# Kernel tuning notes

Hardware: AMD Instinct MI355X
Metric: run time of the kernel (lower is better)

The kernel has to match this reference:

```python
import jax, jax.numpy as jnp
import numpy as np

N_NODES = 50000


def gcn_conv(x, edge_index, W, b, n):
    # PyG GCNConv: xW, add self-loops, symmetric degree normalization,
    # scatter-add messages from source (row) to target (col).
    xw = x @ W
    row, col = edge_index[0], edge_index[1]
    loops = jnp.arange(n, dtype=edge_index.dtype)
    row = jnp.concatenate([row, loops])
    col = jnp.concatenate([col, loops])
    deg = jax.ops.segment_sum(jnp.ones(row.shape[0], dtype=xw.dtype), col, num_segments=n)
    dinv = jnp.where(deg > 0, jax.lax.rsqrt(deg), 0.0)
    norm = dinv[row] * dinv[col]  # [E+N]
    out = jax.ops.segment_sum(xw[row] * norm[:, None], col, num_segments=n)
    return out + b


def setup_inputs() -> dict:
    key = jax.random.key(0)
    ks = jax.random.split(key, 5)
    n, d_in, d_h, d_out, n_edges = N_NODES, 128, 128, 4, 600000
    x = jax.random.normal(ks[0], (n, d_in), dtype=jnp.float32)
    edge_index = jax.random.randint(ks[1], (2, n_edges), 0, n, dtype=jnp.int64)
    W1 = jax.random.normal(ks[2], (d_in, d_h), dtype=jnp.float32) * (1.0 / np.sqrt(d_in))
    b1 = jnp.zeros((d_h,), dtype=jnp.float32)
    W2 = jax.random.normal(ks[3], (d_h, d_h), dtype=jnp.float32) * (1.0 / np.sqrt(d_h))
    b2 = jnp.zeros((d_h,), dtype=jnp.float32)
    Wfc = jax.random.normal(ks[4], (2 * d_h, d_out), dtype=jnp.float32) * (1.0 / np.sqrt(2 * d_h))
    bfc = jnp.zeros((d_out,), dtype=jnp.float32)
    return {"x": x, "edge_index": edge_index, "W1": W1, "b1": b1,
            "W2": W2, "b2": b2, "Wfc": Wfc, "bfc": bfc}


def reference(x, edge_index, W1, b1, W2, b2, Wfc, bfc):
    n = x.shape[0]
    # dropout is identity at inference (training=False)
    h = jax.nn.relu(gcn_conv(x, edge_index, W1, b1, n))
    h = jax.nn.relu(gcn_conv(h, edge_index, W2, b2, n))
    # edge-level gather + concat + linear classifier
    edge_x = jnp.concatenate([h[edge_index[0]], h[edge_index[1]]], axis=-1)  # [E, 2*d_h]
    edge_scores = edge_x @ Wfc + bfc  # [E, d_out]
    return jax.nn.log_softmax(edge_scores, axis=1)
```

## Files before the change

### kernel.cpp

```cpp
#include <hip/hip_runtime.h>
#include <math.h>
#include <stdint.h>

#define D 128
#define SCAN_CHUNK 2048
#define LDA 136

typedef __attribute__((ext_vector_type(8))) short v8s;
typedef __attribute__((ext_vector_type(4))) float v4f;

static __device__ __forceinline__ uint16_t f2bf(float f) {
    uint32_t u = __float_as_uint(f);
    u = (u + 0x7fff + ((u >> 16) & 1)) >> 16;
    return (uint16_t)u;
}
static __device__ __forceinline__ float bf2f(uint16_t h) { return __uint_as_float((uint32_t)h << 16); }
static __device__ __forceinline__ float bf_lo(uint32_t u) { return __uint_as_float(u << 16); }
static __device__ __forceinline__ float bf_hi(uint32_t u) { return __uint_as_float(u & 0xffff0000u); }


__global__ void countpack_kernel(const int* __restrict__ col, int* __restrict__ cnt,
                                 int* __restrict__ rnk, int E,
                                 const float* __restrict__ W1, const float* __restrict__ W2,
                                 uint16_t* __restrict__ Wh, uint16_t* __restrict__ Wl) {
    int tid = blockIdx.x * blockDim.x + threadIdx.x;
    if (tid < 2 * 16384) {
        int layer = tid >> 14;
        int li = tid & 16383;
        int j = li & 7, lane = (li >> 3) & 63, f = li >> 9;
        int kstep = f >> 3, tile = f & 7;
        int k = kstep * 32 + ((lane >> 4) * 8) + j;
        int nn = tile * 16 + (lane & 15);
        const float* W = layer ? W2 : W1;
        float v = W[k * 128 + nn];
        uint16_t h = f2bf(v);
        Wh[tid] = h;
        Wl[tid] = f2bf(v - bf2f(h));
    }
    if (tid < E) rnk[tid] = atomicAdd(&cnt[col[tid]], 1);
}


__global__ __launch_bounds__(256) void scanA_kernel(const int* __restrict__ cnt,
                                                    int* __restrict__ bsum,
                                                    float* __restrict__ dinv, int n) {
    __shared__ int wsum[4];
    int b = blockIdx.x, t = threadIdx.x;
    int base = b * SCAN_CHUNK;
    int s = 0;
#pragma unroll
    for (int k = 0; k < SCAN_CHUNK / 256; k++) {
        int i = base + k * 256 + t;
        if (i < n) {
            int c = cnt[i];
            s += c;
            dinv[i] = rsqrtf((float)c + 1.0f);
        }
    }
#pragma unroll
    for (int off = 32; off > 0; off >>= 1) s += __shfl_xor(s, off, 64);
    if ((t & 63) == 0) wsum[t >> 6] = s;
    __syncthreads();
    if (t == 0) bsum[b] = wsum[0] + wsum[1] + wsum[2] + wsum[3];
}


__global__ __launch_bounds__(256) void scanC_kernel(const int* __restrict__ cnt,
                                                    const int* __restrict__ bsum,
                                                    int* __restrict__ offs, int n, int nb) {
    __shared__ int stage[SCAN_CHUNK];
    __shared__ int res[SCAN_CHUNK];
    __shared__ int tsum[256];
    __shared__ int sb[64];
    int b = blockIdx.x, t = threadIdx.x;
    if (t < 64) {
        int v = (t < nb) ? bsum[t] : 0;
        int inc = v;
#pragma unroll
        for (int off = 1; off < 64; off <<= 1) {
            int u = __shfl_up(inc, off, 64);
            if (t >= off) inc += u;
        }
        sb[t] = inc;
    }
    int base = b * SCAN_CHUNK;
#pragma unroll
    for (int k = 0; k < SCAN_CHUNK / 256; k++) {
        int i = base + k * 256 + t;
        stage[k * 256 + t] = (i < n) ? cnt[i] : 0;
    }
    __syncthreads();
    int my = 0;
#pragma unroll
    for (int j = 0; j < 8; j++) my += stage[t * 8 + j];
    tsum[t] = my;
    __syncthreads();
    for (int off = 1; off < 256; off <<= 1) {
        int v = (t >= off) ? tsum[t - off] : 0;
        __syncthreads();
        tsum[t] += v;
        __syncthreads();
    }
    int bbase = (b == 0) ? 0 : sb[b - 1];
    int run = tsum[t] - my + bbase;
#pragma unroll
    for (int j = 0; j < 8; j++) {
        res[t * 8 + j] = run;
        run += stage[t * 8 + j];
    }
    __syncthreads();
#pragma unroll
    for (int k = 0; k < SCAN_CHUNK / 256; k++) {
        int i = base + k * 256 + t;
        if (i < n) offs[i] = res[k * 256 + t];
    }
    if (b == gridDim.x - 1 && t == 0) offs[n] = sb[nb - 1];
}


static __device__ __forceinline__ void gemm_body(const uint16_t Ah[][LDA],
                                                 const uint16_t Al[][LDA],
                                                 const uint16_t* __restrict__ Wph,
                                                 const uint16_t* __restrict__ Wpl,
                                                 const float* __restrict__ dinv,
                                                 uint16_t* __restrict__ Cb,
                                                 int base_row, int M, int t) {
    int lane = t & 63, w = t >> 6;
    int m_l = lane & 15, quad = lane >> 4;
    int arow = w * 16 + m_l;

    v4f acc[8];
#pragma unroll
    for (int i = 0; i < 8; i++) acc[i] = (v4f){0.f, 0.f, 0.f, 0.f};

#pragma unroll
    for (int ks = 0; ks < 4; ks++) {
        v8s ah = *(const v8s*)&Ah[arow][ks * 32 + quad * 8];
        v8s al = *(const v8s*)&Al[arow][ks * 32 + quad * 8];
#pragma unroll
        for (int ti = 0; ti < 8; ti++) {
            int f = ks * 8 + ti;
            v8s bh = *(const v8s*)(Wph + ((size_t)(f * 64 + lane)) * 8);
            v8s bl = *(const v8s*)(Wpl + ((size_t)(f * 64 + lane)) * 8);
            acc[ti] = __builtin_amdgcn_mfma_f32_16x16x32_bf16(al, bh, acc[ti], 0, 0, 0);
            acc[ti] = __builtin_amdgcn_mfma_f32_16x16x32_bf16(ah, bl, acc[ti], 0, 0, 0);
            acc[ti] = __builtin_amdgcn_mfma_f32_16x16x32_bf16(ah, bh, acc[ti], 0, 0, 0);
        }
    }

    int rbase = base_row + w * 16 + quad * 4;
#pragma unroll
    for (int reg = 0; reg < 4; reg++) {
        int gr = rbase + reg;
        if (gr < M) {
            float di = dinv[gr];
#pragma unroll
            for (int ti = 0; ti < 8; ti++) {
                Cb[(size_t)gr * D + ti * 16 + m_l] = f2bf(di * acc[ti][reg]);
            }
        }
    }
}


__global__ __launch_bounds__(256) void fillgemm_kernel(const int* __restrict__ row,
                                                       const int* __restrict__ col,
                                                       const int* __restrict__ rnk,
                                                       const int* __restrict__ offs,
                                                       int* __restrict__ adj, int E,
                                                       const float* __restrict__ A,
                                                       const uint16_t* __restrict__ Wph,
                                                       const uint16_t* __restrict__ Wpl,
                                                       const float* __restrict__ dinv,
                                                       uint16_t* __restrict__ Cb, int M,
                                                       int nbG) {
    __shared__ uint16_t Ah[64][LDA];
    __shared__ uint16_t Al[64][LDA];
    int t = threadIdx.x;

    if (blockIdx.x >= nbG) {
        int e = (blockIdx.x - nbG) * 256 + t;
        if (e < E) adj[offs[col[e]] + rnk[e]] = row[e];
        return;
    }

    int base_row = blockIdx.x * 64;
#pragma unroll
    for (int kk = 0; kk < 8; kk++) {
        int idx = kk * 256 + t;
        int r = idx >> 5;
        int c4 = idx & 31;
        int gr = base_row + r;
        float4 f = (gr < M) ? *(const float4*)(A + (size_t)gr * D + c4 * 4)
                            : make_float4(0.f, 0.f, 0.f, 0.f);
        uint16_t h0 = f2bf(f.x), h1 = f2bf(f.y), h2 = f2bf(f.z), h3 = f2bf(f.w);
        uint16_t l0 = f2bf(f.x - bf2f(h0)), l1 = f2bf(f.y - bf2f(h1));
        uint16_t l2 = f2bf(f.z - bf2f(h2)), l3 = f2bf(f.w - bf2f(h3));
        *(ushort4*)&Ah[r][c4 * 4] = make_ushort4(h0, h1, h2, h3);
        *(ushort4*)&Al[r][c4 * 4] = make_ushort4(l0, l1, l2, l3);
    }
    __syncthreads();
    gemm_body(Ah, Al, Wph, Wpl, dinv, Cb, base_row, M, t);
}


__global__ __launch_bounds__(256) void agggemm_kernel(const uint32_t* __restrict__ xwb,
                                                      const int* __restrict__ adj,
                                                      const int* __restrict__ offs,
                                                      const float* __restrict__ dinv,
                                                      const float* __restrict__ bias,
                                                      const uint16_t* __restrict__ Wph,
                                                      const uint16_t* __restrict__ Wpl,
                                                      uint16_t* __restrict__ Cb, int M) {
    __shared__ uint16_t Ah[64][LDA];
    __shared__ uint16_t Al[64][LDA];
    int t = threadIdx.x, lane = t & 63, w = t >> 6;
    int base_row = blockIdx.x * 64;
    float2 bv = ((const float2*)bias)[lane];

    for (int rr = 0; rr < 8; rr++) {
        int rA = w * 16 + rr, rB = rA + 8;
        int iA = base_row + rA, iB = base_row + rB;
        float a0 = 0.f, a1 = 0.f, c0 = 0.f, c1 = 0.f;
        int jA = 0, eA = 0, jB = 0, eB = 0;
        if (iA < M) {
            uint32_t su = xwb[(size_t)iA * (D / 2) + lane];
            a0 = bf_lo(su); a1 = bf_hi(su);
            jA = offs[iA]; eA = offs[iA + 1];
        }
        if (iB < M) {
            uint32_t su = xwb[(size_t)iB * (D / 2) + lane];
            c0 = bf_lo(su); c1 = bf_hi(su);
            jB = offs[iB]; eB = offs[iB + 1];
        }
        while (jA + 7 < eA && jB + 7 < eB) {
            int xx[8], yy[8];
#pragma unroll
            for (int q = 0; q < 8; q++) { xx[q] = adj[jA + q]; yy[q] = adj[jB + q]; }
            uint32_t uA[8], uB[8];
#pragma unroll
            for (int q = 0; q < 8; q++) {
                uA[q] = xwb[(size_t)xx[q] * (D / 2) + lane];
                uB[q] = xwb[(size_t)yy[q] * (D / 2) + lane];
            }
#pragma unroll
            for (int q = 0; q < 8; q++) {
                a0 += bf_lo(uA[q]); a1 += bf_hi(uA[q]);
                c0 += bf_lo(uB[q]); c1 += bf_hi(uB[q]);
            }
            jA += 8; jB += 8;
        }
        for (; jA + 7 < eA; jA += 8) {
            int xx[8]; uint32_t uA[8];
#pragma unroll
            for (int q = 0; q < 8; q++) xx[q] = adj[jA + q];
#pragma unroll
            for (int q = 0; q < 8; q++) uA[q] = xwb[(size_t)xx[q] * (D / 2) + lane];
#pragma unroll
            for (int q = 0; q < 8; q++) { a0 += bf_lo(uA[q]); a1 += bf_hi(uA[q]); }
        }
        for (; jA + 3 < eA; jA += 4) {
            int x0 = adj[jA], x1 = adj[jA + 1], x2 = adj[jA + 2], x3 = adj[jA + 3];
            uint32_t u0 = xwb[(size_t)x0 * (D / 2) + lane];
            uint32_t u1 = xwb[(size_t)x1 * (D / 2) + lane];
            uint32_t u2 = xwb[(size_t)x2 * (D / 2) + lane];
            uint32_t u3 = xwb[(size_t)x3 * (D / 2) + lane];
            a0 += bf_lo(u0); a1 += bf_hi(u0);
            a0 += bf_lo(u1); a1 += bf_hi(u1);
            a0 += bf_lo(u2); a1 += bf_hi(u2);
            a0 += bf_lo(u3); a1 += bf_hi(u3);
        }
        for (; jA < eA; jA++) {
            uint32_t u = xwb[(size_t)adj[jA] * (D / 2) + lane];
            a0 += bf_lo(u); a1 += bf_hi(u);
        }
        for (; jB + 7 < eB; jB += 8) {
            int yy[8]; uint32_t uB[8];
#pragma unroll
            for (int q = 0; q < 8; q++) yy[q] = adj[jB + q];
#pragma unroll
            for (int q = 0; q < 8; q++) uB[q] = xwb[(size_t)yy[q] * (D / 2) + lane];
#pragma unroll
            for (int q = 0; q < 8; q++) { c0 += bf_lo(uB[q]); c1 += bf_hi(uB[q]); }
        }
        for (; jB + 3 < eB; jB += 4) {
            int y0 = adj[jB], y1 = adj[jB + 1], y2 = adj[jB + 2], y3 = adj[jB + 3];
            uint32_t u0 = xwb[(size_t)y0 * (D / 2) + lane];
            uint32_t u1 = xwb[(size_t)y1 * (D / 2) + lane];
            uint32_t u2 = xwb[(size_t)y2 * (D / 2) + lane];
            uint32_t u3 = xwb[(size_t)y3 * (D / 2) + lane];
            c0 += bf_lo(u0); c1 += bf_hi(u0);
            c0 += bf_lo(u1); c1 += bf_hi(u1);
            c0 += bf_lo(u2); c1 += bf_hi(u2);
            c0 += bf_lo(u3); c1 += bf_hi(u3);
        }
        for (; jB < eB; jB++) {
            uint32_t u = xwb[(size_t)adj[jB] * (D / 2) + lane];
            c0 += bf_lo(u); c1 += bf_hi(u);
        }
        float diA = (iA < M) ? dinv[iA] : 0.f;
        float diB = (iB < M) ? dinv[iB] : 0.f;
        float oA0 = fmaxf(fmaf(diA, a0, bv.x), 0.f);
        float oA1 = fmaxf(fmaf(diA, a1, bv.y), 0.f);
        float oB0 = fmaxf(fmaf(diB, c0, bv.x), 0.f);
        float oB1 = fmaxf(fmaf(diB, c1, bv.y), 0.f);
        if (iA >= M) { oA0 = 0.f; oA1 = 0.f; }
        if (iB >= M) { oB0 = 0.f; oB1 = 0.f; }
        uint16_t hA0 = f2bf(oA0), hA1 = f2bf(oA1);
        uint16_t lA0 = f2bf(oA0 - bf2f(hA0)), lA1 = f2bf(oA1 - bf2f(hA1));
        uint16_t hB0 = f2bf(oB0), hB1 = f2bf(oB1);
        uint16_t lB0 = f2bf(oB0 - bf2f(hB0)), lB1 = f2bf(oB1 - bf2f(hB1));
        *(ushort2*)&Ah[rA][2 * lane] = make_ushort2(hA0, hA1);
        *(ushort2*)&Al[rA][2 * lane] = make_ushort2(lA0, lA1);
        *(ushort2*)&Ah[rB][2 * lane] = make_ushort2(hB0, hB1);
        *(ushort2*)&Al[rB][2 * lane] = make_ushort2(lB0, lB1);
    }
    __syncthreads();
    gemm_body(Ah, Al, Wph, Wpl, dinv, Cb, base_row, M, t);
}


__global__ __launch_bounds__(256) void agg2pq_kernel(const uint32_t* __restrict__ xwb,
                                                     const int* __restrict__ adj,
                                                     const int* __restrict__ offs,
                                                     const float* __restrict__ dinv,
                                                     const float* __restrict__ bias,
                                                     const float* __restrict__ Wfc,
                                                     const float* __restrict__ bfc,
                                                     float* __restrict__ P1,
                                                     float* __restrict__ P2, int n) {
    int wave = (int)((blockIdx.x * (size_t)blockDim.x + threadIdx.x) >> 6);
    int lane = threadIdx.x & 63;
    if (wave >= n) return;
    int i = wave;
    uint32_t su = xwb[(size_t)i * (D / 2) + lane];
    float acc0 = bf_lo(su);
    float acc1 = bf_hi(su);
    int s = offs[i], e = offs[i + 1];
    int j = s;
    for (; j + 7 < e; j += 8) {
        int r0 = adj[j],     r1 = adj[j + 1], r2 = adj[j + 2], r3 = adj[j + 3];
        int r4 = adj[j + 4], r5 = adj[j + 5], r6 = adj[j + 6], r7 = adj[j + 7];
        uint32_t u0 = xwb[(size_t)r0 * (D / 2) + lane];
        uint32_t u1 = xwb[(size_t)r1 * (D / 2) + lane];
        uint32_t u2 = xwb[(size_t)r2 * (D / 2) + lane];
        uint32_t u3 = xwb[(size_t)r3 * (D / 2) + lane];
        uint32_t u4 = xwb[(size_t)r4 * (D / 2) + lane];
        uint32_t u5 = xwb[(size_t)r5 * (D / 2) + lane];
        uint32_t u6 = xwb[(size_t)r6 * (D / 2) + lane];
        uint32_t u7 = xwb[(size_t)r7 * (D / 2) + lane];
        acc0 += bf_lo(u0); acc1 += bf_hi(u0);
        acc0 += bf_lo(u1); acc1 += bf_hi(u1);
        acc0 += bf_lo(u2); acc1 += bf_hi(u2);
        acc0 += bf_lo(u3); acc1 += bf_hi(u3);
        acc0 += bf_lo(u4); acc1 += bf_hi(u4);
        acc0 += bf_lo(u5); acc1 += bf_hi(u5);
        acc0 += bf_lo(u6); acc1 += bf_hi(u6);
        acc0 += bf_lo(u7); acc1 += bf_hi(u7);
    }
    for (; j + 3 < e; j += 4) {
        int r0 = adj[j], r1 = adj[j + 1], r2 = adj[j + 2], r3 = adj[j + 3];
        uint32_t u0 = xwb[(size_t)r0 * (D / 2) + lane];
        uint32_t u1 = xwb[(size_t)r1 * (D / 2) + lane];
        uint32_t u2 = xwb[(size_t)r2 * (D / 2) + lane];
        uint32_t u3 = xwb[(size_t)r3 * (D / 2) + lane];
        acc0 += bf_lo(u0); acc1 += bf_hi(u0);
        acc0 += bf_lo(u1); acc1 += bf_hi(u1);
        acc0 += bf_lo(u2); acc1 += bf_hi(u2);
        acc0 += bf_lo(u3); acc1 += bf_hi(u3);
    }
    for (; j < e; j++) {
        int r = adj[j];
        uint32_t u = xwb[(size_t)r * (D / 2) + lane];
        acc0 += bf_lo(u); acc1 += bf_hi(u);
    }
    float di = dinv[i];
    float2 bv = ((const float2*)bias)[lane];
    float o0 = fmaxf(fmaf(di, acc0, bv.x), 0.f);
    float o1 = fmaxf(fmaf(di, acc1, bv.y), 0.f);

    const float4* W4 = (const float4*)Wfc;
    float4 wa = W4[2 * lane];
    float4 wb = W4[2 * lane + 1];
    float4 wc = W4[128 + 2 * lane];
    float4 wd = W4[129 + 2 * lane];
    float p0 = fmaf(o0, wa.x, o1 * wb.x), p1 = fmaf(o0, wa.y, o1 * wb.y);
    float p2 = fmaf(o0, wa.z, o1 * wb.z), p3 = fmaf(o0, wa.w, o1 * wb.w);
    float q0 = fmaf(o0, wc.x, o1 * wd.x), q1 = fmaf(o0, wc.y, o1 * wd.y);
    float q2 = fmaf(o0, wc.z, o1 * wd.z), q3 = fmaf(o0, wc.w, o1 * wd.w);
#pragma unroll
    for (int off = 1; off < 64; off <<= 1) {
        p0 += __shfl_xor(p0, off, 64);
        p1 += __shfl_xor(p1, off, 64);
        p2 += __shfl_xor(p2, off, 64);
        p3 += __shfl_xor(p3, off, 64);
        q0 += __shfl_xor(q0, off, 64);
        q1 += __shfl_xor(q1, off, 64);
        q2 += __shfl_xor(q2, off, 64);
        q3 += __shfl_xor(q3, off, 64);
    }
    if (lane == 0) {
        float4 bb = *(const float4*)bfc;
        *(float4*)(P1 + (size_t)i * 4) = make_float4(p0 + bb.x, p1 + bb.y, p2 + bb.z, p3 + bb.w);
        *(float4*)(P2 + (size_t)i * 4) = make_float4(q0, q1, q2, q3);
    }
}


__global__ __launch_bounds__(256) void edge2_kernel(const int* __restrict__ row,
                                                    const int* __restrict__ col,
                                                    const float* __restrict__ P1,
                                                    const float* __restrict__ P2,
                                                    float* __restrict__ out, int E) {
    int e = blockIdx.x * blockDim.x + threadIdx.x;
    if (e >= E) return;
    int r = row[e], c = col[e];
    float4 a = ((const float4*)P1)[r];
    float4 b = ((const float4*)P2)[c];
    float sx = a.x + b.x, sy = a.y + b.y, sz = a.z + b.z, sw = a.w + b.w;
    float m = fmaxf(fmaxf(sx, sy), fmaxf(sz, sw));
    float e0 = expf(sx - m), e1 = expf(sy - m), e2 = expf(sz - m), e3 = expf(sw - m);
    float lse = m + logf(e0 + e1 + e2 + e3);
    *(float4*)(out + (size_t)e * 4) = make_float4(sx - lse, sy - lse, sz - lse, sw - lse);
}


extern "C" void kernel_launch(void* const* d_in, const int* in_sizes, int n_in,
                              void* d_out, int out_size, void* d_ws, size_t ws_size,
                              hipStream_t stream) {
    const float* x   = (const float*)d_in[0];
    const int*   ei  = (const int*)d_in[1];
    const float* W1  = (const float*)d_in[2];
    const float* b1  = (const float*)d_in[3];
    const float* W2  = (const float*)d_in[4];
    const float* b2  = (const float*)d_in[5];
    const float* Wfc = (const float*)d_in[6];
    const float* bfc = (const float*)d_in[7];
    float* out = (float*)d_out;

    int n = in_sizes[0] / D;
    int E = in_sizes[1] / 2;
    const int* row = ei;
    const int* col = ei + E;

    int nbScan = (n + SCAN_CHUNK - 1) / SCAN_CHUNK;

    uint16_t* xwb  = (uint16_t*)d_ws;
    uint16_t* xwb2 = xwb + (size_t)n * D;
    int*      cnt  = (int*)(xwb2 + (size_t)n * D);
    int*      offs = cnt + n;
    int*      bsum = offs + (n + 4);
    int*      adj  = bsum + 64;
    int*      rnk  = adj + E;
    float*    dinv = (float*)(rnk + E);
    uint16_t* Wph  = (uint16_t*)(dinv + n);
    uint16_t* Wpl  = Wph + 2 * 16384;
    float*    P1   = (float*)(Wpl + 2 * 16384);
    float*    P2   = P1 + (size_t)n * 4;

    int nb_e = (E + 255) / 256;
    int nbG  = (n + 63) / 64;

    hipMemsetAsync(cnt, 0, (size_t)n * sizeof(int), stream);
    countpack_kernel<<<nb_e, 256, 0, stream>>>(col, cnt, rnk, E, W1, W2, Wph, Wpl);
    scanA_kernel<<<nbScan, 256, 0, stream>>>(cnt, bsum, dinv, n);
    scanC_kernel<<<nbScan, 256, 0, stream>>>(cnt, bsum, offs, n, nbScan);

    fillgemm_kernel<<<nbG + nb_e, 256, 0, stream>>>(row, col, rnk, offs, adj, E,
                                                    x, Wph, Wpl, dinv, xwb, n, nbG);

    agggemm_kernel<<<nbG, 256, 0, stream>>>((const uint32_t*)xwb, adj, offs, dinv, b1,
                                            Wph + 16384, Wpl + 16384, xwb2, n);

    agg2pq_kernel<<<(n + 3) / 4, 256, 0, stream>>>((const uint32_t*)xwb2, adj, offs, dinv, b2,
                                                   Wfc, bfc, P1, P2, n);

    edge2_kernel<<<nb_e, 256, 0, stream>>>(row, col, P1, P2, out, E);
}
```

Baseline: 235.7 us.

## Split feature dimension into quarter tables for cache-local gather aggregation

The GEMM output changes to a quarter-blocked layout of four 32-column slabs, each n×32 bf16, so each aggregation pass gathers from a smaller table that fits in L2 cache. Aggregation splits into persistent grid-stride kernels, with block index mapped to a quarter. Layer 1 aggregation now writes fp32 h1 to a separate buffer, and a standalone gemm2 kernel consumes it. Layer 2 aggregation accumulates the classifier projections into P1/P2 with atomics, after scanA pre-initialises them with the bias and zeros. This adds an fp32 intermediate round trip, an extra launch and atomic traffic, in exchange for better gather locality.

```diff
diff --git a/kernel.cpp b/kernel.cpp
--- a/kernel.cpp
+++ b/kernel.cpp
@@ -5,6 +5,8 @@
 #define D 128
 #define SCAN_CHUNK 2048
 #define LDA 136
+#define AGG_BLOCKS 4096
+#define AGG_STRIDE 4096
 
 typedef __attribute__((ext_vector_type(8))) short v8s;
 typedef __attribute__((ext_vector_type(4))) float v4f;
@@ -43,10 +45,14 @@
 
 __global__ __launch_bounds__(256) void scanA_kernel(const int* __restrict__ cnt,
                                                     int* __restrict__ bsum,
-                                                    float* __restrict__ dinv, int n) {
+                                                    float* __restrict__ dinv,
+                                                    const float* __restrict__ bfc,
+                                                    float* __restrict__ P1,
+                                                    float* __restrict__ P2, int n) {
     __shared__ int wsum[4];
     int b = blockIdx.x, t = threadIdx.x;
     int base = b * SCAN_CHUNK;
+    float4 bb = *(const float4*)bfc;
     int s = 0;
 #pragma unroll
     for (int k = 0; k < SCAN_CHUNK / 256; k++) {
@@ -55,6 +61,8 @@
             int c = cnt[i];
             s += c;
             dinv[i] = rsqrtf((float)c + 1.0f);
+            ((float4*)P1)[i] = bb;
+            ((float4*)P2)[i] = make_float4(0.f, 0.f, 0.f, 0.f);
         }
     }
 #pragma unroll
@@ -156,7 +164,8 @@
             float di = dinv[gr];
 #pragma unroll
             for (int ti = 0; ti < 8; ti++) {
-                Cb[(size_t)gr * D + ti * 16 + m_l] = f2bf(di * acc[ti][reg]);
+                Cb[(((size_t)(ti >> 1)) * M + gr) * 32 + (ti & 1) * 16 + m_l] =
+                    f2bf(di * acc[ti][reg]);
             }
         }
     }
@@ -204,205 +213,151 @@
 }
 
 
-__global__ __launch_bounds__(256) void agggemm_kernel(const uint32_t* __restrict__ xwb,
-                                                      const int* __restrict__ adj,
-                                                      const int* __restrict__ offs,
-                                                      const float* __restrict__ dinv,
-                                                      const float* __restrict__ bias,
-                                                      const uint16_t* __restrict__ Wph,
-                                                      const uint16_t* __restrict__ Wpl,
-                                                      uint16_t* __restrict__ Cb, int M) {
+__global__ __launch_bounds__(256) void gemm2_kernel(const float* __restrict__ h1q,
+                                                    const uint16_t* __restrict__ Wph,
+                                                    const uint16_t* __restrict__ Wpl,
+                                                    const float* __restrict__ dinv,
+                                                    uint16_t* __restrict__ Cb, int M) {
     __shared__ uint16_t Ah[64][LDA];
     __shared__ uint16_t Al[64][LDA];
-    int t = threadIdx.x, lane = t & 63, w = t >> 6;
+    int t = threadIdx.x;
     int base_row = blockIdx.x * 64;
-    float2 bv = ((const float2*)bias)[lane];
-
-    for (int rr = 0; rr < 8; rr++) {
-        int rA = w * 16 + rr, rB = rA + 8;
-        int iA = base_row + rA, iB = base_row + rB;
-        float a0 = 0.f, a1 = 0.f, c0 = 0.f, c1 = 0.f;
-        int jA = 0, eA = 0, jB = 0, eB = 0;
-        if (iA < M) {
-            uint32_t su = xwb[(size_t)iA * (D / 2) + lane];
-            a0 = bf_lo(su); a1 = bf_hi(su);
-            jA = offs[iA]; eA = offs[iA + 1];
-        }
-        if (iB < M) {
-            uint32_t su = xwb[(size_t)iB * (D / 2) + lane];
-            c0 = bf_lo(su); c1 = bf_hi(su);
-            jB = offs[iB]; eB = offs[iB + 1];
-        }
-        while (jA + 7 < eA && jB + 7 < eB) {
-            int xx[8], yy[8];
-#pragma unroll
-            for (int q = 0; q < 8; q++) { xx[q] = adj[jA + q]; yy[q] = adj[jB + q]; }
-            uint32_t uA[8], uB[8];
-#pragma unroll
-            for (int q = 0; q < 8; q++) {
-                uA[q] = xwb[(size_t)xx[q] * (D / 2) + lane];
-                uB[q] = xwb[(size_t)yy[q] * (D / 2) + lane];
-            }
-#pragma unroll
-            for (int q = 0; q < 8; q++) {
-                a0 += bf_lo(uA[q]); a1 += bf_hi(uA[q]);
-                c0 += bf_lo(uB[q]); c1 += bf_hi(uB[q]);
-            }
-            jA += 8; jB += 8;
-        }
-        for (; jA + 7 < eA; jA += 8) {
-            int xx[8]; uint32_t uA[8];
-#pragma unroll
-            for (int q = 0; q < 8; q++) xx[q] = adj[jA + q];
-#pragma unroll
-            for (int q = 0; q < 8; q++) uA[q] = xwb[(size_t)xx[q] * (D / 2) + lane];
-#pragma unroll
-            for (int q = 0; q < 8; q++) { a0 += bf_lo(uA[q]); a1 += bf_hi(uA[q]); }
-        }
-        for (; jA + 3 < eA; jA += 4) {
-            int x0 = adj[jA], x1 = adj[jA + 1], x2 = adj[jA + 2], x3 = adj[jA + 3];
-            uint32_t u0 = xwb[(size_t)x0 * (D / 2) + lane];
-            uint32_t u1 = xwb[(size_t)x1 * (D / 2) + lane];
-            uint32_t u2 = xwb[(size_t)x2 * (D / 2) + lane];
-            uint32_t u3 = xwb[(size_t)x3 * (D / 2) + lane];
-            a0 += bf_lo(u0); a1 += bf_hi(u0);
+#pragma unroll
+    for (int kk = 0; kk < 8; kk++) {
+        int idx = kk * 256 + t;
+        int r = idx >> 5;
+        int c4 = idx & 31;
+        int gr = base_row + r;
+        int qq = c4 >> 3, cc = c4 & 7;
+        float4 f = (gr < M) ? ((const float4*)h1q)[((size_t)qq * M + gr) * 8 + cc]
+                            : make_float4(0.f, 0.f, 0.f, 0.f);
+        uint16_t h0 = f2bf(f.x), h1 = f2bf(f.y), h2 = f2bf(f.z), h3 = f2bf(f.w);
+        uint16_t l0 = f2bf(f.x - bf2f(h0)), l1 = f2bf(f.y - bf2f(h1));
+        uint16_t l2 = f2bf(f.z - bf2f(h2)), l3 = f2bf(f.w - bf2f(h3));
+        *(ushort4*)&Ah[r][c4 * 4] = make_ushort4(h0, h1, h2, h3);
+        *(ushort4*)&Al[r][c4 * 4] = make_ushort4(l0, l1, l2, l3);
+    }
+    __syncthreads();
+    gemm_body(Ah, Al, Wph, Wpl, dinv, Cb, base_row, M, t);
+}
+
+
+__global__ __launch_bounds__(256) void aggq1_kernel(const uint32_t* __restrict__ xwbq,
+                                                    const int* __restrict__ adj,
+                                                    const int* __restrict__ offs,
+                                                    const float* __restrict__ dinv,
+                                                    const float* __restrict__ bias,
+                                                    float* __restrict__ h1q, int n) {
+    int b = blockIdx.x, t = threadIdx.x;
+    int q = (b & 7) >> 1;
+    int sub = ((b >> 3) << 1) + (b & 1);
+    int w = t >> 6, lane = t & 63;
+    int c = lane & 15, e = lane >> 4;
+    const uint32_t* tbl = xwbq + (size_t)q * n * 16;
+    float2 bv = ((const float2*)bias)[q * 16 + c];
+    for (int i = sub * 4 + w; i < n; i += AGG_STRIDE) {
+        uint32_t su = tbl[(size_t)i * 16 + c];
+        float a0 = (e == 0) ? bf_lo(su) : 0.f;
+        float a1 = (e == 0) ? bf_hi(su) : 0.f;
+        int j = offs[i], en = offs[i + 1];
+        for (; j + 7 < en; j += 8) {
+            int i1 = adj[j + e], i2 = adj[j + 4 + e];
+            uint32_t u1 = tbl[(size_t)i1 * 16 + c];
+            uint32_t u2 = tbl[(size_t)i2 * 16 + c];
+            a0 += bf_lo(u1) + bf_lo(u2);
+            a1 += bf_hi(u1) + bf_hi(u2);
+        }
+        for (; j + 3 < en; j += 4) {
+            int i1 = adj[j + e];
+            uint32_t u1 = tbl[(size_t)i1 * 16 + c];
             a0 += bf_lo(u1); a1 += bf_hi(u1);
-            a0 += bf_lo(u2); a1 += bf_hi(u2);
-            a0 += bf_lo(u3); a1 += bf_hi(u3);
-        }
-        for (; jA < eA; jA++) {
-            uint32_t u = xwb[(size_t)adj[jA] * (D / 2) + lane];
-            a0 += bf_lo(u); a1 += bf_hi(u);
-        }
-        for (; jB + 7 < eB; jB += 8) {
-            int yy[8]; uint32_t uB[8];
-#pragma unroll
-            for (int q = 0; q < 8; q++) yy[q] = adj[jB + q];
-#pragma unroll
-            for (int q = 0; q < 8; q++) uB[q] = xwb[(size_t)yy[q] * (D / 2) + lane];
-#pragma unroll
-            for (int q = 0; q < 8; q++) { c0 += bf_lo(uB[q]); c1 += bf_hi(uB[q]); }
-        }
-        for (; jB + 3 < eB; jB += 4) {
-            int y0 = adj[jB], y1 = adj[jB + 1], y2 = adj[jB + 2], y3 = adj[jB + 3];
-            uint32_t u0 = xwb[(size_t)y0 * (D / 2) + lane];
-            uint32_t u1 = xwb[(size_t)y1 * (D / 2) + lane];
-            uint32_t u2 = xwb[(size_t)y2 * (D / 2) + lane];
-            uint32_t u3 = xwb[(size_t)y3 * (D / 2) + lane];
-            c0 += bf_lo(u0); c1 += bf_hi(u0);
-            c0 += bf_lo(u1); c1 += bf_hi(u1);
-            c0 += bf_lo(u2); c1 += bf_hi(u2);
-            c0 += bf_lo(u3); c1 += bf_hi(u3);
-        }
-        for (; jB < eB; jB++) {
-            uint32_t u = xwb[(size_t)adj[jB] * (D / 2) + lane];
-            c0 += bf_lo(u); c1 += bf_hi(u);
-        }
-        float diA = (iA < M) ? dinv[iA] : 0.f;
-        float diB = (iB < M) ? dinv[iB] : 0.f;
-        float oA0 = fmaxf(fmaf(diA, a0, bv.x), 0.f);
-        float oA1 = fmaxf(fmaf(diA, a1, bv.y), 0.f);
-        float oB0 = fmaxf(fmaf(diB, c0, bv.x), 0.f);
-        float oB1 = fmaxf(fmaf(diB, c1, bv.y), 0.f);
-        if (iA >= M) { oA0 = 0.f; oA1 = 0.f; }
-        if (iB >= M) { oB0 = 0.f; oB1 = 0.f; }
-        uint16_t hA0 = f2bf(oA0), hA1 = f2bf(oA1);
-        uint16_t lA0 = f2bf(oA0 - bf2f(hA0)), lA1 = f2bf(oA1 - bf2f(hA1));
-        uint16_t hB0 = f2bf(oB0), hB1 = f2bf(oB1);
-        uint16_t lB0 = f2bf(oB0 - bf2f(hB0)), lB1 = f2bf(oB1 - bf2f(hB1));
-        *(ushort2*)&Ah[rA][2 * lane] = make_ushort2(hA0, hA1);
-        *(ushort2*)&Al[rA][2 * lane] = make_ushort2(lA0, lA1);
-        *(ushort2*)&Ah[rB][2 * lane] = make_ushort2(hB0, hB1);
-        *(ushort2*)&Al[rB][2 * lane] = make_ushort2(lB0, lB1);
-    }
-    __syncthreads();
-    gemm_body(Ah, Al, Wph, Wpl, dinv, Cb, base_row, M, t);
-}
-
-
-__global__ __launch_bounds__(256) void agg2pq_kernel(const uint32_t* __restrict__ xwb,
-                                                     const int* __restrict__ adj,
-                                                     const int* __restrict__ offs,
-                                                     const float* __restrict__ dinv,
-                                                     const float* __restrict__ bias,
-                                                     const float* __restrict__ Wfc,
-                                                     const float* __restrict__ bfc,
-                                                     float* __restrict__ P1,
-                                                     float* __restrict__ P2, int n) {
-    int wave = (int)((blockIdx.x * (size_t)blockDim.x + threadIdx.x) >> 6);
-    int lane = threadIdx.x & 63;
-    if (wave >= n) return;
-    int i = wave;
-    uint32_t su = xwb[(size_t)i * (D / 2) + lane];
-    float acc0 = bf_lo(su);
-    float acc1 = bf_hi(su);
-    int s = offs[i], e = offs[i + 1];
-    int j = s;
-    for (; j + 7 < e; j += 8) {
-        int r0 = adj[j],     r1 = adj[j + 1], r2 = adj[j + 2], r3 = adj[j + 3];
-        int r4 = adj[j + 4], r5 = adj[j + 5], r6 = adj[j + 6], r7 = adj[j + 7];
-        uint32_t u0 = xwb[(size_t)r0 * (D / 2) + lane];
-        uint32_t u1 = xwb[(size_t)r1 * (D / 2) + lane];
-        uint32_t u2 = xwb[(size_t)r2 * (D / 2) + lane];
-        uint32_t u3 = xwb[(size_t)r3 * (D / 2) + lane];
-        uint32_t u4 = xwb[(size_t)r4 * (D / 2) + lane];
-        uint32_t u5 = xwb[(size_t)r5 * (D / 2) + lane];
-        uint32_t u6 = xwb[(size_t)r6 * (D / 2) + lane];
-        uint32_t u7 = xwb[(size_t)r7 * (D / 2) + lane];
-        acc0 += bf_lo(u0); acc1 += bf_hi(u0);
-        acc0 += bf_lo(u1); acc1 += bf_hi(u1);
-        acc0 += bf_lo(u2); acc1 += bf_hi(u2);
-        acc0 += bf_lo(u3); acc1 += bf_hi(u3);
-        acc0 += bf_lo(u4); acc1 += bf_hi(u4);
-        acc0 += bf_lo(u5); acc1 += bf_hi(u5);
-        acc0 += bf_lo(u6); acc1 += bf_hi(u6);
-        acc0 += bf_lo(u7); acc1 += bf_hi(u7);
-    }
-    for (; j + 3 < e; j += 4) {
-        int r0 = adj[j], r1 = adj[j + 1], r2 = adj[j + 2], r3 = adj[j + 3];
-        uint32_t u0 = xwb[(size_t)r0 * (D / 2) + lane];
-        uint32_t u1 = xwb[(size_t)r1 * (D / 2) + lane];
-        uint32_t u2 = xwb[(size_t)r2 * (D / 2) + lane];
-        uint32_t u3 = xwb[(size_t)r3 * (D / 2) + lane];
-        acc0 += bf_lo(u0); acc1 += bf_hi(u0);
-        acc0 += bf_lo(u1); acc1 += bf_hi(u1);
-        acc0 += bf_lo(u2); acc1 += bf_hi(u2);
-        acc0 += bf_lo(u3); acc1 += bf_hi(u3);
-    }
-    for (; j < e; j++) {
-        int r = adj[j];
-        uint32_t u = xwb[(size_t)r * (D / 2) + lane];
-        acc0 += bf_lo(u); acc1 += bf_hi(u);
-    }
-    float di = dinv[i];
-    float2 bv = ((const float2*)bias)[lane];
-    float o0 = fmaxf(fmaf(di, acc0, bv.x), 0.f);
-    float o1 = fmaxf(fmaf(di, acc1, bv.y), 0.f);
-
+        }
+        if (j + e < en) {
+            uint32_t u1 = tbl[(size_t)adj[j + e] * 16 + c];
+            a0 += bf_lo(u1); a1 += bf_hi(u1);
+        }
+        a0 += __shfl_xor(a0, 16, 64); a0 += __shfl_xor(a0, 32, 64);
+        a1 += __shfl_xor(a1, 16, 64); a1 += __shfl_xor(a1, 32, 64);
+        float di = dinv[i];
+        float o0 = fmaxf(fmaf(di, a0, bv.x), 0.f);
+        float o1 = fmaxf(fmaf(di, a1, bv.y), 0.f);
+        if (lane < 16)
+            ((float2*)h1q)[((size_t)q * n + i) * 16 + c] = make_float2(o0, o1);
+    }
+}
+
+
+__global__ __launch_bounds__(256) void aggq2_kernel(const uint32_t* __restrict__ xwbq,
+                                                    const int* __restrict__ adj,
+                                                    const int* __restrict__ offs,
+                                                    const float* __restrict__ dinv,
+                                                    const float* __restrict__ bias,
+                                                    const float* __restrict__ Wfc,
+                                                    float* __restrict__ P1,
+                                                    float* __restrict__ P2, int n) {
+    int b = blockIdx.x, t = threadIdx.x;
+    int q = (b & 7) >> 1;
+    int sub = ((b >> 3) << 1) + (b & 1);
+    int w = t >> 6, lane = t & 63;
+    int c = lane & 15, e = lane >> 4;
+    const uint32_t* tbl = xwbq + (size_t)q * n * 16;
+    float2 bv = ((const float2*)bias)[q * 16 + c];
     const float4* W4 = (const float4*)Wfc;
-    float4 wa = W4[2 * lane];
-    float4 wb = W4[2 * lane + 1];
-    float4 wc = W4[128 + 2 * lane];
-    float4 wd = W4[129 + 2 * lane];
-    float p0 = fmaf(o0, wa.x, o1 * wb.x), p1 = fmaf(o0, wa.y, o1 * wb.y);
-    float p2 = fmaf(o0, wa.z, o1 * wb.z), p3 = fmaf(o0, wa.w, o1 * wb.w);
-    float q0 = fmaf(o0, wc.x, o1 * wd.x), q1 = fmaf(o0, wc.y, o1 * wd.y);
-    float q2 = fmaf(o0, wc.z, o1 * wd.z), q3 = fmaf(o0, wc.w, o1 * wd.w);
-#pragma unroll
-    for (int off = 1; off < 64; off <<= 1) {
-        p0 += __shfl_xor(p0, off, 64);
-        p1 += __shfl_xor(p1, off, 64);
-        p2 += __shfl_xor(p2, off, 64);
-        p3 += __shfl_xor(p3, off, 64);
-        q0 += __shfl_xor(q0, off, 64);
-        q1 += __shfl_xor(q1, off, 64);
-        q2 += __shfl_xor(q2, off, 64);
-        q3 += __shfl_xor(q3, off, 64);
-    }
-    if (lane == 0) {
-        float4 bb = *(const float4*)bfc;
-        *(float4*)(P1 + (size_t)i * 4) = make_float4(p0 + bb.x, p1 + bb.y, p2 + bb.z, p3 + bb.w);
-        *(float4*)(P2 + (size_t)i * 4) = make_float4(q0, q1, q2, q3);
+    float4 w1a = W4[q * 32 + 2 * c];
+    float4 w1b = W4[q * 32 + 2 * c + 1];
+    float4 w2a = W4[128 + q * 32 + 2 * c];
+    float4 w2b = W4[128 + q * 32 + 2 * c + 1];
+    for (int i = sub * 4 + w; i < n; i += AGG_STRIDE) {
+        uint32_t su = tbl[(size_t)i * 16 + c];
+        float a0 = (e == 0) ? bf_lo(su) : 0.f;
+        float a1 = (e == 0) ? bf_hi(su) : 0.f;
+        int j = offs[i], en = offs[i + 1];
+        for (; j + 7 < en; j += 8) {
+            int i1 = adj[j + e], i2 = adj[j + 4 + e];
+            uint32_t u1 = tbl[(size_t)i1 * 16 + c];
+            uint32_t u2 = tbl[(size_t)i2 * 16 + c];
+            a0 += bf_lo(u1) + bf_lo(u2);
+            a1 += bf_hi(u1) + bf_hi(u2);
+        }
+        for (; j + 3 < en; j += 4) {
+            int i1 = adj[j + e];
+            uint32_t u1 = tbl[(size_t)i1 * 16 + c];
+            a0 += bf_lo(u1); a1 += bf_hi(u1);
+        }
+        if (j + e < en) {
+            uint32_t u1 = tbl[(size_t)adj[j + e] * 16 + c];
+            a0 += bf_lo(u1); a1 += bf_hi(u1);
+        }
+        a0 += __shfl_xor(a0, 16, 64); a0 += __shfl_xor(a0, 32, 64);
+        a1 += __shfl_xor(a1, 16, 64); a1 += __shfl_xor(a1, 32, 64);
+        float di = dinv[i];
+        float o0 = fmaxf(fmaf(di, a0, bv.x), 0.f);
+        float o1 = fmaxf(fmaf(di, a1, bv.y), 0.f);
+        float p0 = fmaf(o0, w1a.x, o1 * w1b.x), p1 = fmaf(o0, w1a.y, o1 * w1b.y);
+        float p2 = fmaf(o0, w1a.z, o1 * w1b.z), p3 = fmaf(o0, w1a.w, o1 * w1b.w);
+        float q0 = fmaf(o0, w2a.x, o1 * w2b.x), q1 = fmaf(o0, w2a.y, o1 * w2b.y);
+        float q2 = fmaf(o0, w2a.z, o1 * w2b.z), q3 = fmaf(o0, w2a.w, o1 * w2b.w);
+#pragma unroll
+        for (int off = 1; off < 16; off <<= 1) {
+            p0 += __shfl_xor(p0, off, 64);
+            p1 += __shfl_xor(p1, off, 64);
+            p2 += __shfl_xor(p2, off, 64);
+            p3 += __shfl_xor(p3, off, 64);
+            q0 += __shfl_xor(q0, off, 64);
+            q1 += __shfl_xor(q1, off, 64);
+            q2 += __shfl_xor(q2, off, 64);
+            q3 += __shfl_xor(q3, off, 64);
+        }
+        if (lane == 0) {
+            atomicAdd(&P1[(size_t)i * 4 + 0], p0);
+            atomicAdd(&P1[(size_t)i * 4 + 1], p1);
+            atomicAdd(&P1[(size_t)i * 4 + 2], p2);
+            atomicAdd(&P1[(size_t)i * 4 + 3], p3);
+            atomicAdd(&P2[(size_t)i * 4 + 0], q0);
+            atomicAdd(&P2[(size_t)i * 4 + 1], q1);
+            atomicAdd(&P2[(size_t)i * 4 + 2], q2);
+            atomicAdd(&P2[(size_t)i * 4 + 3], q3);
+        }
     }
 }
 
@@ -447,7 +402,8 @@
 
     uint16_t* xwb  = (uint16_t*)d_ws;
     uint16_t* xwb2 = xwb + (size_t)n * D;
-    int*      cnt  = (int*)(xwb2 + (size_t)n * D);
+    float*    h1q  = (float*)(xwb2 + (size_t)n * D);
+    int*      cnt  = (int*)(h1q + (size_t)n * D);
     int*      offs = cnt + n;
     int*      bsum = offs + (n + 4);
     int*      adj  = bsum + 64;
@@ -463,17 +419,19 @@
 
     hipMemsetAsync(cnt, 0, (size_t)n * sizeof(int), stream);
     countpack_kernel<<<nb_e, 256, 0, stream>>>(col, cnt, rnk, E, W1, W2, Wph, Wpl);
-    scanA_kernel<<<nbScan, 256, 0, stream>>>(cnt, bsum, dinv, n);
+    scanA_kernel<<<nbScan, 256, 0, stream>>>(cnt, bsum, dinv, bfc, P1, P2, n);
     scanC_kernel<<<nbScan, 256, 0, stream>>>(cnt, bsum, offs, n, nbScan);
 
     fillgemm_kernel<<<nbG + nb_e, 256, 0, stream>>>(row, col, rnk, offs, adj, E,
                                                     x, Wph, Wpl, dinv, xwb, n, nbG);
 
-    agggemm_kernel<<<nbG, 256, 0, stream>>>((const uint32_t*)xwb, adj, offs, dinv, b1,
-                                            Wph + 16384, Wpl + 16384, xwb2, n);
-
-    agg2pq_kernel<<<(n + 3) / 4, 256, 0, stream>>>((const uint32_t*)xwb2, adj, offs, dinv, b2,
-                                                   Wfc, bfc, P1, P2, n);
+    aggq1_kernel<<<AGG_BLOCKS, 256, 0, stream>>>((const uint32_t*)xwb, adj, offs, dinv, b1,
+                                                 h1q, n);
+
+    gemm2_kernel<<<nbG, 256, 0, stream>>>(h1q, Wph + 16384, Wpl + 16384, dinv, xwb2, n);
+
+    aggq2_kernel<<<AGG_BLOCKS, 256, 0, stream>>>((const uint32_t*)xwb2, adj, offs, dinv, b2,
+                                                 Wfc, P1, P2, n);
 
     edge2_kernel<<<nb_e, 256, 0, stream>>>(row, col, P1, P2, out, E);
 }
```

Result: slower. 347.6 us (+47.5%).
